# Kernel optimization log

Hardware: AMD Instinct MI355X
Metric: run time of the kernel (lower is better)

## Reference

```python
import jax, jax.numpy as jnp
import numpy as np

N_NODES = 100000
N_EDGES = 1600000
IN_CH = 128
OUT_CH = 64


def setup_inputs() -> dict:
    key = jax.random.key(0)
    k1, k2, k3 = jax.random.split(key, 3)
    x = jax.random.normal(k1, (N_NODES, IN_CH), dtype=jnp.float32)
    edge_index = jax.random.randint(k2, (2, N_EDGES), 0, N_NODES, dtype=jnp.int64)
    # Glorot-style init for the GCN weight, zero bias (PyG defaults)
    W = jax.random.normal(k3, (IN_CH, OUT_CH), dtype=jnp.float32) * (1.0 / np.sqrt(IN_CH))
    b = jnp.zeros((OUT_CH,), dtype=jnp.float32)
    return {"x": x, "edge_index": edge_index, "W": W, "b": b}


def reference(x, edge_index, W, b):
    n = x.shape[0]
    # add self loops (GCNConv default add_self_loops=True)
    loop = jnp.arange(n, dtype=edge_index.dtype)
    row = jnp.concatenate([edge_index[0], loop])  # source
    col = jnp.concatenate([edge_index[1], loop])  # target
    # symmetric degree normalization on augmented graph
    deg = jax.ops.segment_sum(jnp.ones_like(col, dtype=x.dtype), col, num_segments=n)
    dinv = jnp.where(deg > 0, jax.lax.rsqrt(deg), 0.0)
    norm = dinv[row] * dinv[col]  # [E+N]
    # linear transform first (out_channels < in_channels), then gather-scale-scatter
    h = x @ W  # [N, OUT]
    msgs = h[row] * norm[:, None]  # [E+N, OUT]
    out = jax.ops.segment_sum(msgs, col, num_segments=n)  # [N, OUT]
    return out + b
```

## Files before the change

### kernel.cpp

```cpp
#include <hip/hip_runtime.h>
#include <hip/hip_bf16.h>


#define IN_CH 128
#define OUT_CH 64
#define BSHIFT 7
#define BNODES 128
#define MAX_NB 800
#define CH_EDGES 7168
#define SORT_CAP 4096
#define XSTR 136

typedef short bf16x8 __attribute__((ext_vector_type(8)));
typedef float f32x4  __attribute__((ext_vector_type(4)));

__device__ __forceinline__ unsigned short f2b(float f) {
    unsigned int u = __float_as_uint(f);
    return (unsigned short)((u + 0x7FFFu + ((u >> 16) & 1u)) >> 16);
}

__global__ __launch_bounds__(256) void wprep_kernel(const float* __restrict__ W,
                                                    unsigned short* __restrict__ wbt,
                                                    int* __restrict__ bucket_cnt,
                                                    int NB) {
    int t = blockIdx.x * 256 + threadIdx.x;
    int k = t >> 6, nn = t & 63;
    wbt[nn * IN_CH + k] = f2b(W[t]);
    if (t < NB) bucket_cnt[t] = 0;
}

__global__ __launch_bounds__(1024) void count_kernel(const int* __restrict__ col,
                                                     int* __restrict__ bucket_cnt,
                                                     int E, int NB) {
    __shared__ int h[MAX_NB];
    int tid = threadIdx.x;
    for (int i = tid; i < NB; i += 1024) h[i] = 0;
    __syncthreads();
    int e0 = blockIdx.x * CH_EDGES;
    #pragma unroll
    for (int r = 0; r < CH_EDGES / 1024; ++r) {
        int e = e0 + r * 1024 + tid;
        if (e < E) atomicAdd(&h[col[e] >> BSHIFT], 1);
    }
    __syncthreads();
    for (int i = tid; i < NB; i += 1024)
        if (h[i]) atomicAdd(&bucket_cnt[i], h[i]);
}

__global__ __launch_bounds__(1024) void scanB_kernel(const int* __restrict__ bucket_cnt,
                                                     int* __restrict__ bucket_start,
                                                     int* __restrict__ cursor,
                                                     int NB, int E) {
    __shared__ int s[1024];
    int tid = threadIdx.x;
    int v   = (tid < NB) ? bucket_cnt[tid] : 0;
    s[tid] = v; __syncthreads();
    #pragma unroll
    for (int off = 1; off < 1024; off <<= 1) {
        int t = (tid >= off) ? s[tid - off] : 0;
        __syncthreads();
        s[tid] += t;
        __syncthreads();
    }
    if (tid < NB) {
        int excl = s[tid] - v;
        bucket_start[tid] = excl;
        cursor[tid] = excl;
    }
    if (tid == 0) bucket_start[NB] = E;
}

__global__ __launch_bounds__(1024) void place_kernel(const int* __restrict__ row,
                                                     const int* __restrict__ col,
                                                     int* __restrict__ cursor,
                                                     int* __restrict__ pairs,
                                                     int E, int NB) {
    __shared__ int h[MAX_NB];
    int tid = threadIdx.x;
    for (int i = tid; i < NB; i += 1024) h[i] = 0;
    __syncthreads();
    int e0 = blockIdx.x * CH_EDGES;
    #pragma unroll
    for (int r1 = 0; r1 < CH_EDGES / 1024; ++r1) {
        int e = e0 + r1 * 1024 + tid;
        if (e < E) atomicAdd(&h[col[e] >> BSHIFT], 1);
    }
    __syncthreads();
    for (int i = tid; i < NB; i += 1024) {
        int c = h[i];
        if (c) h[i] = atomicAdd(&cursor[i], c);
    }
    __syncthreads();
    #pragma unroll
    for (int r2 = 0; r2 < CH_EDGES / 1024; ++r2) {
        int e = e0 + r2 * 1024 + tid;
        if (e < E) {
            int c = col[e];
            int b = c >> BSHIFT;
            int pos = atomicAdd(&h[b], 1);
            pairs[pos] = row[e] | ((c & (BNODES - 1)) << 17);
        }
    }
}

__global__ __launch_bounds__(256) void bucket_sort_kernel(
    const int* __restrict__ bucket_start, const int* __restrict__ pairs,
    int* __restrict__ csr_row, int* __restrict__ row_start,
    float* __restrict__ dinv, int n, int E)
{
    __shared__ int cnt[BNODES];
    __shared__ int deg[BNODES];
    __shared__ int cur[BNODES];
    __shared__ int sorted[SORT_CAP];

    int b = blockIdx.x, tid = threadIdx.x;
    int node0 = b << BSHIFT;
    int nodeCnt = min(BNODES, n - node0);
    int s0 = bucket_start[b], s1 = bucket_start[b + 1];
    int m = s1 - s0;

    if (tid < BNODES) cnt[tid] = 0;
    __syncthreads();
    for (int e = s0 + tid; e < s1; e += 256) atomicAdd(&cnt[pairs[e] >> 17], 1);
    __syncthreads();
    if (tid < BNODES) deg[tid] = cnt[tid];
    __syncthreads();
    #pragma unroll
    for (int off = 1; off < BNODES; off <<= 1) {
        int t = (tid >= off && tid < BNODES) ? cnt[tid - off] : 0;
        __syncthreads();
        if (tid < BNODES) cnt[tid] += t;
        __syncthreads();
    }
    if (tid < BNODES) {
        int excl = cnt[tid] - deg[tid];
        cur[tid] = excl;
        if (tid < nodeCnt) {
            row_start[node0 + tid] = s0 + excl;
            dinv[node0 + tid] = rsqrtf((float)(deg[tid] + 1));
        }
    }
    if (b == gridDim.x - 1 && tid == 0) row_start[n] = E;
    __syncthreads();

    if (m <= SORT_CAP) {
        for (int e = s0 + tid; e < s1; e += 256) {
            int p   = pairs[e];
            int pos = atomicAdd(&cur[p >> 17], 1);
            sorted[pos] = p & 0x1FFFF;
        }
        __syncthreads();
        for (int i = tid; i < m; i += 256) csr_row[s0 + i] = sorted[i];
    } else {
        if (tid < BNODES) cur[tid] += s0;
        __syncthreads();
        for (int e = s0 + tid; e < s1; e += 256) {
            int p   = pairs[e];
            int pos = atomicAdd(&cur[p >> 17], 1);
            csr_row[pos] = p & 0x1FFFF;
        }
    }
}

__global__ __launch_bounds__(256) void gemm_kernel(
    const float* __restrict__ x, const unsigned short* __restrict__ wbt,
    const float* __restrict__ dinv, unsigned short* __restrict__ hpb, int n)
{
    __shared__ __align__(16) unsigned short xl[64 * XSTR];
    __shared__ __align__(16) unsigned short wl[64 * XSTR];

    int tid  = threadIdx.x;
    int row0 = blockIdx.x * 64;

    {
        const uint4* src = (const uint4*)wbt;
        #pragma unroll
        for (int i = 0; i < 4; ++i) {
            int flat = tid + i * 256;
            int nn = flat >> 4, c = flat & 15;
            *(uint4*)(wl + nn * XSTR + c * 8) = src[flat];
        }
    }
    #pragma unroll
    for (int i = 0; i < 4; ++i) {
        int r  = (tid >> 4) + i * 16;
        int c  = tid & 15;
        int gr = row0 + r;
        float4 v0 = make_float4(0.f,0.f,0.f,0.f), v1 = v0;
        float d = 0.f;
        if (gr < n) {
            d = dinv[gr];
            const float4* xr = (const float4*)(x + (size_t)gr * IN_CH);
            v0 = xr[c * 2]; v1 = xr[c * 2 + 1];
        }
        uint4 p;
        p.x = ((unsigned)f2b(v0.y * d) << 16) | f2b(v0.x * d);
        p.y = ((unsigned)f2b(v0.w * d) << 16) | f2b(v0.z * d);
        p.z = ((unsigned)f2b(v1.y * d) << 16) | f2b(v1.x * d);
        p.w = ((unsigned)f2b(v1.w * d) << 16) | f2b(v1.z * d);
        *(uint4*)(xl + r * XSTR + c * 8) = p;
    }
    __syncthreads();

    int lane = tid & 63, w = tid >> 6;
    int mrow = lane & 15;
    int g    = lane >> 4;

    f32x4 acc0 = {0,0,0,0}, acc1 = {0,0,0,0}, acc2 = {0,0,0,0}, acc3 = {0,0,0,0};
    const unsigned short* xbase = xl + (w * 16 + mrow) * XSTR + g * 8;
    const unsigned short* wbase = wl + mrow * XSTR + g * 8;

    #pragma unroll
    for (int k4 = 0; k4 < 4; ++k4) {
        bf16x8 a  = *(const bf16x8*)(xbase + k4 * 32);
        bf16x8 b0 = *(const bf16x8*)(wbase +             k4 * 32);
        bf16x8 b1 = *(const bf16x8*)(wbase + 16 * XSTR + k4 * 32);
        bf16x8 b2 = *(const bf16x8*)(wbase + 32 * XSTR + k4 * 32);
        bf16x8 b3 = *(const bf16x8*)(wbase + 48 * XSTR + k4 * 32);
        acc0 = __builtin_amdgcn_mfma_f32_16x16x32_bf16(a, b0, acc0, 0, 0, 0);
        acc1 = __builtin_amdgcn_mfma_f32_16x16x32_bf16(a, b1, acc1, 0, 0, 0);
        acc2 = __builtin_amdgcn_mfma_f32_16x16x32_bf16(a, b2, acc2, 0, 0, 0);
        acc3 = __builtin_amdgcn_mfma_f32_16x16x32_bf16(a, b3, acc3, 0, 0, 0);
    }
    __syncthreads();

    {
        int cm = g * 4;
        #pragma unroll
        for (int r = 0; r < 4; ++r) {
            unsigned short* crow = xl + (w * 16 + cm + r) * XSTR + mrow;
            crow[ 0] = f2b(acc0[r]);
            crow[16] = f2b(acc1[r]);
            crow[32] = f2b(acc2[r]);
            crow[48] = f2b(acc3[r]);
        }
    }
    __syncthreads();
    #pragma unroll
    for (int i = 0; i < 2; ++i) {
        int flat = tid + i * 256;
        int r = flat >> 3, c = flat & 7;
        int gr = row0 + r;
        if (gr < n) {
            uint4 v = *(const uint4*)(xl + r * XSTR + c * 8);
            *(uint4*)(hpb + (size_t)gr * OUT_CH + c * 8) = v;
        }
    }
}

__global__ __launch_bounds__(256) void aggregate_kernel(
    const int* __restrict__ row_start, const int* __restrict__ csr_row,
    const unsigned short* __restrict__ hpb, const float* __restrict__ dinv,
    const float* __restrict__ bias, float* __restrict__ out, int n)
{
    int wid  = (blockIdx.x * 256 + threadIdx.x) >> 6;
    int lane = threadIdx.x & 63;
    if (wid >= n) return;
    int half = lane >> 5;
    int hl   = lane & 31;

    const unsigned int* hp32 = (const unsigned int*)hpb;

    int s0 = row_start[wid];
    int s1 = row_start[wid + 1];

    float al0=0.f,al1=0.f,al2=0.f,al3=0.f,al4=0.f,al5=0.f,al6=0.f,al7=0.f;
    float ah0=0.f,ah1=0.f,ah2=0.f,ah3=0.f,ah4=0.f,ah5=0.f,ah6=0.f,ah7=0.f;

    for (int base = s0; base < s1; base += 64) {
        int cnt  = min(64, s1 - base);
        int ridx = (base + lane < s1) ? csr_row[base + lane] : 0;
        for (int j0 = 0; j0 < cnt; j0 += 16) {
            int e0 = j0      + half, e1 = j0 +  2 + half;
            int e2 = j0 +  4 + half, e3 = j0 +  6 + half;
            int e4 = j0 +  8 + half, e5 = j0 + 10 + half;
            int e6 = j0 + 12 + half, e7 = j0 + 14 + half;
            int r0 = __shfl(ridx, e0), r1 = __shfl(ridx, e1);
            int r2 = __shfl(ridx, e2), r3 = __shfl(ridx, e3);
            int r4 = __shfl(ridx, e4), r5 = __shfl(ridx, e5);
            int r6 = __shfl(ridx, e6), r7 = __shfl(ridx, e7);
            unsigned v0 = (e0 < cnt) ? hp32[(size_t)r0 * 32 + hl] : 0u;
            unsigned v1 = (e1 < cnt) ? hp32[(size_t)r1 * 32 + hl] : 0u;
            unsigned v2 = (e2 < cnt) ? hp32[(size_t)r2 * 32 + hl] : 0u;
            unsigned v3 = (e3 < cnt) ? hp32[(size_t)r3 * 32 + hl] : 0u;
            unsigned v4 = (e4 < cnt) ? hp32[(size_t)r4 * 32 + hl] : 0u;
            unsigned v5 = (e5 < cnt) ? hp32[(size_t)r5 * 32 + hl] : 0u;
            unsigned v6 = (e6 < cnt) ? hp32[(size_t)r6 * 32 + hl] : 0u;
            unsigned v7 = (e7 < cnt) ? hp32[(size_t)r7 * 32 + hl] : 0u;
            al0 += __uint_as_float(v0 << 16); ah0 += __uint_as_float(v0 & 0xFFFF0000u);
            al1 += __uint_as_float(v1 << 16); ah1 += __uint_as_float(v1 & 0xFFFF0000u);
            al2 += __uint_as_float(v2 << 16); ah2 += __uint_as_float(v2 & 0xFFFF0000u);
            al3 += __uint_as_float(v3 << 16); ah3 += __uint_as_float(v3 & 0xFFFF0000u);
            al4 += __uint_as_float(v4 << 16); ah4 += __uint_as_float(v4 & 0xFFFF0000u);
            al5 += __uint_as_float(v5 << 16); ah5 += __uint_as_float(v5 & 0xFFFF0000u);
            al6 += __uint_as_float(v6 << 16); ah6 += __uint_as_float(v6 & 0xFFFF0000u);
            al7 += __uint_as_float(v7 << 16); ah7 += __uint_as_float(v7 & 0xFFFF0000u);
        }
    }
    float sl = ((al0 + al1) + (al2 + al3)) + ((al4 + al5) + (al6 + al7));
    float sh = ((ah0 + ah1) + (ah2 + ah3)) + ((ah4 + ah5) + (ah6 + ah7));
    sl += __shfl_xor(sl, 32);
    sh += __shfl_xor(sh, 32);

    if (half == 0) {
        unsigned int sv = hp32[(size_t)wid * 32 + hl];
        sl += __uint_as_float(sv << 16);
        sh += __uint_as_float(sv & 0xFFFF0000u);
        float d = dinv[wid];
        float2 bb = ((const float2*)bias)[hl];
        float2 o;
        o.x = fmaf(d, sl, bb.x);
        o.y = fmaf(d, sh, bb.y);
        ((float2*)(out + (size_t)wid * OUT_CH))[hl] = o;
    }
}

extern "C" void kernel_launch(void* const* d_in, const int* in_sizes, int n_in,
                              void* d_out, int out_size, void* d_ws, size_t ws_size,
                              hipStream_t stream) {
    const float* x  = (const float*)d_in[0];
    const int*   ei = (const int*)d_in[1];
    const float* W  = (const float*)d_in[2];
    const float* b  = (const float*)d_in[3];
    float*       out = (float*)d_out;

    int n = in_sizes[0] / IN_CH;
    int E = in_sizes[1] / 2;
    const int* row = ei;
    const int* col = ei + E;

    int NB   = (n + BNODES - 1) >> BSHIFT;
    int NBLK = (E + CH_EDGES - 1) / CH_EDGES;

    char* ws = (char*)d_ws;
    int*   bucket_cnt   = (int*)ws;   ws += (size_t)NB * 4;
    int*   bucket_start = (int*)ws;   ws += (size_t)(NB + 1) * 4;
    int*   cursor       = (int*)ws;   ws += (size_t)NB * 4;
    int*   row_start    = (int*)ws;   ws += (size_t)(n + 1) * 4;
    float* dinv         = (float*)ws; ws += (size_t)n * 4;
    int*   csr_row      = (int*)ws;   ws += (size_t)E * 4;
    unsigned short* wbt = (unsigned short*)ws; ws += (size_t)IN_CH * OUT_CH * 2;
    ws = (char*)(((uintptr_t)ws + 255) & ~(uintptr_t)255);
    int*            pairs = (int*)ws;
    unsigned short* hpb   = (unsigned short*)ws;

    wprep_kernel      <<<(IN_CH * OUT_CH) / 256, 256, 0, stream>>>(W, wbt, bucket_cnt, NB);
    count_kernel      <<<NBLK, 1024, 0, stream>>>(col, bucket_cnt, E, NB);
    scanB_kernel      <<<1, 1024, 0, stream>>>(bucket_cnt, bucket_start, cursor, NB, E);
    place_kernel      <<<NBLK, 1024, 0, stream>>>(row, col, cursor, pairs, E, NB);
    bucket_sort_kernel<<<NB, 256, 0, stream>>>(bucket_start, pairs, csr_row, row_start, dinv, n, E);
    gemm_kernel       <<<(n + 63) / 64, 256, 0, stream>>>(x, wbt, dinv, hpb, n);
    aggregate_kernel  <<<(n + 3) / 4, 256, 0, stream>>>(row_start, csr_row, hpb, dinv, b, out, n);
}
```

Measured before the change: 181.2 us.

## Use fixed-stride buckets and a sentinel-padded CSR to drop count and scan kernels

Each destination bucket now gets a fixed slot of PSTRIDE entries, so the separate edge-count and bucket-scan kernels go away and place_kernel writes directly from cursors seeded at t*PSTRIDE. Each node's adjacency is padded to a multiple of 8 with a sentinel index n, which points at an extra hpb row written by the GEMM. The aggregation loop can then run fixed rounds of 4 gathers per half-wave with no bounds checks, using a single packed row_info word (start | rounds<<22). The cost is more workspace and extra padded gathers. Correctness also depends on no bucket exceeding PSTRIDE entries and on the sentinel row being zero.

```diff
diff --git a/kernel.cpp b/kernel.cpp
--- a/kernel.cpp
+++ b/kernel.cpp
@@ -9,6 +9,7 @@
 #define MAX_NB 800
 #define CH_EDGES 7168
 #define SORT_CAP 4096
+#define PSTRIDE 4096
 #define XSTR 136
 
 typedef short bf16x8 __attribute__((ext_vector_type(8)));
@@ -21,53 +22,12 @@
 
 __global__ __launch_bounds__(256) void wprep_kernel(const float* __restrict__ W,
                                                     unsigned short* __restrict__ wbt,
-                                                    int* __restrict__ bucket_cnt,
+                                                    int* __restrict__ cursor,
                                                     int NB) {
     int t = blockIdx.x * 256 + threadIdx.x;
     int k = t >> 6, nn = t & 63;
     wbt[nn * IN_CH + k] = f2b(W[t]);
-    if (t < NB) bucket_cnt[t] = 0;
-}
-
-__global__ __launch_bounds__(1024) void count_kernel(const int* __restrict__ col,
-                                                     int* __restrict__ bucket_cnt,
-                                                     int E, int NB) {
-    __shared__ int h[MAX_NB];
-    int tid = threadIdx.x;
-    for (int i = tid; i < NB; i += 1024) h[i] = 0;
-    __syncthreads();
-    int e0 = blockIdx.x * CH_EDGES;
-    #pragma unroll
-    for (int r = 0; r < CH_EDGES / 1024; ++r) {
-        int e = e0 + r * 1024 + tid;
-        if (e < E) atomicAdd(&h[col[e] >> BSHIFT], 1);
-    }
-    __syncthreads();
-    for (int i = tid; i < NB; i += 1024)
-        if (h[i]) atomicAdd(&bucket_cnt[i], h[i]);
-}
-
-__global__ __launch_bounds__(1024) void scanB_kernel(const int* __restrict__ bucket_cnt,
-                                                     int* __restrict__ bucket_start,
-                                                     int* __restrict__ cursor,
-                                                     int NB, int E) {
-    __shared__ int s[1024];
-    int tid = threadIdx.x;
-    int v   = (tid < NB) ? bucket_cnt[tid] : 0;
-    s[tid] = v; __syncthreads();
-    #pragma unroll
-    for (int off = 1; off < 1024; off <<= 1) {
-        int t = (tid >= off) ? s[tid - off] : 0;
-        __syncthreads();
-        s[tid] += t;
-        __syncthreads();
-    }
-    if (tid < NB) {
-        int excl = s[tid] - v;
-        bucket_start[tid] = excl;
-        cursor[tid] = excl;
-    }
-    if (tid == 0) bucket_start[NB] = E;
+    if (t < NB) cursor[t] = t * PSTRIDE;
 }
 
 __global__ __launch_bounds__(1024) void place_kernel(const int* __restrict__ row,
@@ -104,26 +64,34 @@
 }
 
 __global__ __launch_bounds__(256) void bucket_sort_kernel(
-    const int* __restrict__ bucket_start, const int* __restrict__ pairs,
-    int* __restrict__ csr_row, int* __restrict__ row_start,
-    float* __restrict__ dinv, int n, int E)
+    const int* __restrict__ cursor_end, const int* __restrict__ pairs,
+    int* __restrict__ csr, int* __restrict__ row_info,
+    float* __restrict__ dinv, int n)
 {
     __shared__ int cnt[BNODES];
     __shared__ int deg[BNODES];
+    __shared__ int pad8[BNODES];
     __shared__ int cur[BNODES];
     __shared__ int sorted[SORT_CAP];
+    __shared__ int ptot_s;
 
     int b = blockIdx.x, tid = threadIdx.x;
     int node0 = b << BSHIFT;
     int nodeCnt = min(BNODES, n - node0);
-    int s0 = bucket_start[b], s1 = bucket_start[b + 1];
-    int m = s1 - s0;
+    int s0 = b * PSTRIDE;
+    int m  = cursor_end[b] - s0;
 
     if (tid < BNODES) cnt[tid] = 0;
     __syncthreads();
-    for (int e = s0 + tid; e < s1; e += 256) atomicAdd(&cnt[pairs[e] >> 17], 1);
-    __syncthreads();
-    if (tid < BNODES) deg[tid] = cnt[tid];
+    for (int e = tid; e < m; e += 256) atomicAdd(&cnt[pairs[s0 + e] >> 17], 1);
+    __syncthreads();
+    if (tid < BNODES) {
+        int d  = cnt[tid];
+        int p8 = (d + 7) & ~7;
+        deg[tid]  = d;
+        pad8[tid] = p8;
+        cnt[tid]  = p8;
+    }
     __syncthreads();
     #pragma unroll
     for (int off = 1; off < BNODES; off <<= 1) {
@@ -133,31 +101,34 @@
         __syncthreads();
     }
     if (tid < BNODES) {
-        int excl = cnt[tid] - deg[tid];
+        int excl = cnt[tid] - pad8[tid];
         cur[tid] = excl;
         if (tid < nodeCnt) {
-            row_start[node0 + tid] = s0 + excl;
+            row_info[node0 + tid] = (s0 + excl) | ((pad8[tid] >> 3) << 22);
             dinv[node0 + tid] = rsqrtf((float)(deg[tid] + 1));
         }
     }
-    if (b == gridDim.x - 1 && tid == 0) row_start[n] = E;
-    __syncthreads();
-
-    if (m <= SORT_CAP) {
-        for (int e = s0 + tid; e < s1; e += 256) {
-            int p   = pairs[e];
+    if (tid == BNODES - 1) ptot_s = cnt[tid];
+    __syncthreads();
+    int ptot = ptot_s;
+
+    if (ptot <= SORT_CAP) {
+        for (int i = tid; i < ptot; i += 256) sorted[i] = n;
+        __syncthreads();
+        for (int e = tid; e < m; e += 256) {
+            int p   = pairs[s0 + e];
             int pos = atomicAdd(&cur[p >> 17], 1);
             sorted[pos] = p & 0x1FFFF;
         }
         __syncthreads();
-        for (int i = tid; i < m; i += 256) csr_row[s0 + i] = sorted[i];
+        for (int i = tid; i < ptot; i += 256) csr[s0 + i] = sorted[i];
     } else {
-        if (tid < BNODES) cur[tid] += s0;
-        __syncthreads();
-        for (int e = s0 + tid; e < s1; e += 256) {
-            int p   = pairs[e];
+        for (int i = tid; i < ptot; i += 256) csr[s0 + i] = n;
+        __syncthreads();
+        for (int e = tid; e < m; e += 256) {
+            int p   = pairs[s0 + e];
             int pos = atomicAdd(&cur[p >> 17], 1);
-            csr_row[pos] = p & 0x1FFFF;
+            csr[s0 + pos] = p & 0x1FFFF;
         }
     }
 }
@@ -241,7 +212,7 @@
         int flat = tid + i * 256;
         int r = flat >> 3, c = flat & 7;
         int gr = row0 + r;
-        if (gr < n) {
+        if (gr <= n) {
             uint4 v = *(const uint4*)(xl + r * XSTR + c * 8);
             *(uint4*)(hpb + (size_t)gr * OUT_CH + c * 8) = v;
         }
@@ -249,7 +220,7 @@
 }
 
 __global__ __launch_bounds__(256) void aggregate_kernel(
-    const int* __restrict__ row_start, const int* __restrict__ csr_row,
+    const int* __restrict__ row_info, const int* __restrict__ csr,
     const unsigned short* __restrict__ hpb, const float* __restrict__ dinv,
     const float* __restrict__ bias, float* __restrict__ out, int n)
 {
@@ -261,44 +232,29 @@
 
     const unsigned int* hp32 = (const unsigned int*)hpb;
 
-    int s0 = row_start[wid];
-    int s1 = row_start[wid + 1];
-
-    float al0=0.f,al1=0.f,al2=0.f,al3=0.f,al4=0.f,al5=0.f,al6=0.f,al7=0.f;
-    float ah0=0.f,ah1=0.f,ah2=0.f,ah3=0.f,ah4=0.f,ah5=0.f,ah6=0.f,ah7=0.f;
-
-    for (int base = s0; base < s1; base += 64) {
-        int cnt  = min(64, s1 - base);
-        int ridx = (base + lane < s1) ? csr_row[base + lane] : 0;
-        for (int j0 = 0; j0 < cnt; j0 += 16) {
-            int e0 = j0      + half, e1 = j0 +  2 + half;
-            int e2 = j0 +  4 + half, e3 = j0 +  6 + half;
-            int e4 = j0 +  8 + half, e5 = j0 + 10 + half;
-            int e6 = j0 + 12 + half, e7 = j0 + 14 + half;
-            int r0 = __shfl(ridx, e0), r1 = __shfl(ridx, e1);
-            int r2 = __shfl(ridx, e2), r3 = __shfl(ridx, e3);
-            int r4 = __shfl(ridx, e4), r5 = __shfl(ridx, e5);
-            int r6 = __shfl(ridx, e6), r7 = __shfl(ridx, e7);
-            unsigned v0 = (e0 < cnt) ? hp32[(size_t)r0 * 32 + hl] : 0u;
-            unsigned v1 = (e1 < cnt) ? hp32[(size_t)r1 * 32 + hl] : 0u;
-            unsigned v2 = (e2 < cnt) ? hp32[(size_t)r2 * 32 + hl] : 0u;
-            unsigned v3 = (e3 < cnt) ? hp32[(size_t)r3 * 32 + hl] : 0u;
-            unsigned v4 = (e4 < cnt) ? hp32[(size_t)r4 * 32 + hl] : 0u;
-            unsigned v5 = (e5 < cnt) ? hp32[(size_t)r5 * 32 + hl] : 0u;
-            unsigned v6 = (e6 < cnt) ? hp32[(size_t)r6 * 32 + hl] : 0u;
-            unsigned v7 = (e7 < cnt) ? hp32[(size_t)r7 * 32 + hl] : 0u;
-            al0 += __uint_as_float(v0 << 16); ah0 += __uint_as_float(v0 & 0xFFFF0000u);
-            al1 += __uint_as_float(v1 << 16); ah1 += __uint_as_float(v1 & 0xFFFF0000u);
-            al2 += __uint_as_float(v2 << 16); ah2 += __uint_as_float(v2 & 0xFFFF0000u);
-            al3 += __uint_as_float(v3 << 16); ah3 += __uint_as_float(v3 & 0xFFFF0000u);
-            al4 += __uint_as_float(v4 << 16); ah4 += __uint_as_float(v4 & 0xFFFF0000u);
-            al5 += __uint_as_float(v5 << 16); ah5 += __uint_as_float(v5 & 0xFFFF0000u);
-            al6 += __uint_as_float(v6 << 16); ah6 += __uint_as_float(v6 & 0xFFFF0000u);
-            al7 += __uint_as_float(v7 << 16); ah7 += __uint_as_float(v7 & 0xFFFF0000u);
-        }
-    }
-    float sl = ((al0 + al1) + (al2 + al3)) + ((al4 + al5) + (al6 + al7));
-    float sh = ((ah0 + ah1) + (ah2 + ah3)) + ((ah4 + ah5) + (ah6 + ah7));
+    int info = row_info[wid];
+    int s    = info & 0x3FFFFF;
+    int rnds = info >> 22;
+
+    const int* ep = csr + s + half;
+
+    float al0=0.f,ah0=0.f, al1=0.f,ah1=0.f, al2=0.f,ah2=0.f, al3=0.f,ah3=0.f;
+    for (int rr = 0; rr < rnds; ++rr, ep += 8) {
+        int r0 = ep[0];
+        int r1 = ep[2];
+        int r2 = ep[4];
+        int r3 = ep[6];
+        unsigned v0 = hp32[(unsigned)(r0 * 32 + hl)];
+        unsigned v1 = hp32[(unsigned)(r1 * 32 + hl)];
+        unsigned v2 = hp32[(unsigned)(r2 * 32 + hl)];
+        unsigned v3 = hp32[(unsigned)(r3 * 32 + hl)];
+        al0 += __uint_as_float(v0 << 16); ah0 += __uint_as_float(v0 & 0xFFFF0000u);
+        al1 += __uint_as_float(v1 << 16); ah1 += __uint_as_float(v1 & 0xFFFF0000u);
+        al2 += __uint_as_float(v2 << 16); ah2 += __uint_as_float(v2 & 0xFFFF0000u);
+        al3 += __uint_as_float(v3 << 16); ah3 += __uint_as_float(v3 & 0xFFFF0000u);
+    }
+    float sl = (al0 + al1) + (al2 + al3);
+    float sh = (ah0 + ah1) + (ah2 + ah3);
     sl += __shfl_xor(sl, 32);
     sh += __shfl_xor(sh, 32);
 
@@ -333,22 +289,18 @@
     int NBLK = (E + CH_EDGES - 1) / CH_EDGES;
 
     char* ws = (char*)d_ws;
-    int*   bucket_cnt   = (int*)ws;   ws += (size_t)NB * 4;
-    int*   bucket_start = (int*)ws;   ws += (size_t)(NB + 1) * 4;
     int*   cursor       = (int*)ws;   ws += (size_t)NB * 4;
-    int*   row_start    = (int*)ws;   ws += (size_t)(n + 1) * 4;
+    int*   row_info     = (int*)ws;   ws += (size_t)n * 4;
     float* dinv         = (float*)ws; ws += (size_t)n * 4;
-    int*   csr_row      = (int*)ws;   ws += (size_t)E * 4;
     unsigned short* wbt = (unsigned short*)ws; ws += (size_t)IN_CH * OUT_CH * 2;
     ws = (char*)(((uintptr_t)ws + 255) & ~(uintptr_t)255);
-    int*            pairs = (int*)ws;
-    unsigned short* hpb   = (unsigned short*)ws;
-
-    wprep_kernel      <<<(IN_CH * OUT_CH) / 256, 256, 0, stream>>>(W, wbt, bucket_cnt, NB);
-    count_kernel      <<<NBLK, 1024, 0, stream>>>(col, bucket_cnt, E, NB);
-    scanB_kernel      <<<1, 1024, 0, stream>>>(bucket_cnt, bucket_start, cursor, NB, E);
+    int*   pairs        = (int*)ws;   ws += (size_t)NB * PSTRIDE * 4;
+    int*   csr          = (int*)ws;   ws += (size_t)NB * PSTRIDE * 4;
+    unsigned short* hpb = (unsigned short*)ws;
+
+    wprep_kernel      <<<(IN_CH * OUT_CH) / 256, 256, 0, stream>>>(W, wbt, cursor, NB);
     place_kernel      <<<NBLK, 1024, 0, stream>>>(row, col, cursor, pairs, E, NB);
-    bucket_sort_kernel<<<NB, 256, 0, stream>>>(bucket_start, pairs, csr_row, row_start, dinv, n, E);
+    bucket_sort_kernel<<<NB, 256, 0, stream>>>(cursor, pairs, csr, row_info, dinv, n);
     gemm_kernel       <<<(n + 63) / 64, 256, 0, stream>>>(x, wbt, dinv, hpb, n);
-    aggregate_kernel  <<<(n + 3) / 4, 256, 0, stream>>>(row_start, csr_row, hpb, dinv, b, out, n);
-}
+    aggregate_kernel  <<<(n + 3) / 4, 256, 0, stream>>>(row_info, csr, hpb, dinv, b, out, n);
+}
```

Result: faster. 174.2 us (-3.9%).
